# Kernel tuning notes

Measured on AMD Instinct MI355X. Metric: run time of the kernel, lower is better.

Reference implementation:

```python
import jax, jax.numpy as jnp
import numpy as np

NUM_STATES = 16
NUM_CHAINS = 8
NUM_NODES = 5000
NUM_ITERS = 100


def setup_inputs() -> dict:
    key = jax.random.key(0)
    k1, k2, k3, k4 = jax.random.split(key, 4)
    return {
        "unnormalized_state_init": jax.random.normal(k1, (NUM_STATES,), dtype=jnp.float32),
        "unnormalized_chain_weights": jax.random.normal(k2, (1, NUM_NODES, NUM_CHAINS), dtype=jnp.float32),
        "unnormalized_emission_matrix": jax.random.normal(k3, (NUM_STATES, NUM_NODES), dtype=jnp.float32),
        "unnormalized_transition_matrix": jax.random.normal(k4, (NUM_STATES, NUM_STATES), dtype=jnp.float32),
    }


def reference(unnormalized_state_init, unnormalized_chain_weights,
              unnormalized_emission_matrix, unnormalized_transition_matrix):
    T = NUM_ITERS
    # log_transform_params: row-stochastic normalizations in log space
    log_state_init = jax.nn.log_softmax(unnormalized_state_init)                    # (S,)
    log_chain_weights = jax.nn.log_softmax(unnormalized_chain_weights, axis=-1)     # (1,N,C)
    log_emission = jax.nn.log_softmax(unnormalized_emission_matrix, axis=1)         # (S,N)
    log_transition = jax.nn.log_softmax(unnormalized_transition_matrix, axis=1)     # (S,S), rows P(next|prev)

    # log_weights: (S,N,C) = log P(node|state) + log P(chain|node,state)
    log_weights = log_emission[:, :, None] + log_chain_weights

    # HMM forward recursion on hidden-state marginals: h_t[j] = logsumexp_i(h_{t-1}[i] + logT[i,j])
    def step(h, _):
        h_new = jax.scipy.special.logsumexp(h[:, None] + log_transition, axis=0)
        return h_new, h_new

    _, hs = jax.lax.scan(step, log_state_init, None, length=T - 1)
    log_hidden_state_probs = jnp.concatenate([log_state_init[None], hs], axis=0)    # (T,S)

    # (T,S,N,C): broadcast hidden-state marginal into node/chain weights
    log_observed_state_probs_ = log_weights[None] + log_hidden_state_probs[:, :, None, None]

    # logsumexp over states (axis 1) then chains (axis -1) == joint logsumexp over axes (1,3)
    log_observed_state_probs = jax.scipy.special.logsumexp(log_observed_state_probs_, axis=(1, 3))  # (T,N)

    # permute(0,1,3,2): (T,S,C,N)
    log_observed_state_probs_perm = jnp.transpose(log_observed_state_probs_, (0, 1, 3, 2))

    return (log_observed_state_probs, log_observed_state_probs_perm, log_hidden_state_probs)
```

## Files before the change

### kernel.cpp

```cpp
#include <hip/hip_runtime.h>
#include <math.h>

#define S 16
#define C 8
#define N 5000
#define T 100
#define N4 1250

__global__ __launch_bounds__(256) void prep_kernel(const float* __restrict__ u_init,
                                                   const float* __restrict__ u_cw,
                                                   const float* __restrict__ u_e,
                                                   const float* __restrict__ u_T,
                                                   float* __restrict__ ws_le,
                                                   float* __restrict__ ws_lcw,
                                                   float* __restrict__ ws_h,
                                                   float* __restrict__ out_h) {
    const int b = blockIdx.x;
    const int tid = threadIdx.x;

    if (b < 16) {
        const float* row = u_e + b * N;
        __shared__ float red[256];
        float m = -INFINITY;
        for (int n = tid; n < N; n += 256) m = fmaxf(m, row[n]);
        red[tid] = m;
        __syncthreads();
        for (int o = 128; o > 0; o >>= 1) {
            if (tid < o) red[tid] = fmaxf(red[tid], red[tid + o]);
            __syncthreads();
        }
        m = red[0];
        __syncthreads();
        float sum = 0.f;
        for (int n = tid; n < N; n += 256) sum += expf(row[n] - m);
        red[tid] = sum;
        __syncthreads();
        for (int o = 128; o > 0; o >>= 1) {
            if (tid < o) red[tid] += red[tid + o];
            __syncthreads();
        }
        const float lse = m + logf(red[0]);
        for (int n = tid; n < N; n += 256) ws_le[b * N + n] = row[n] - lse;
    } else if (b < 36) {
        const int n = (b - 16) * 256 + tid;
        if (n < N) {
            float v[C];
            float m = -INFINITY;
            for (int c = 0; c < C; ++c) {
                v[c] = u_cw[n * C + c];
                m = fmaxf(m, v[c]);
            }
            float s = 0.f;
            for (int c = 0; c < C; ++c) s += expf(v[c] - m);
            const float lse = m + logf(s);
            for (int c = 0; c < C; ++c) ws_lcw[n * C + c] = v[c] - lse;
        }
    } else {
        if (tid < S) {
            const int j = tid;
            float m = -INFINITY;
            for (int i = 0; i < S; ++i) m = fmaxf(m, u_init[i]);
            float ssum = 0.f;
            for (int i = 0; i < S; ++i) ssum += expf(u_init[i] - m);
            const float lse0 = m + logf(ssum);
            const float h0 = u_init[j] - lse0;
            out_h[j] = h0;
            ws_h[j] = h0;
            float mr = -INFINITY;
            for (int k = 0; k < S; ++k) mr = fmaxf(mr, u_T[j * S + k]);
            float sr = 0.f;
            for (int k = 0; k < S; ++k) sr += expf(u_T[j * S + k] - mr);
            const float lse_row = mr + logf(sr);
            float texp[S];
            #pragma unroll
            for (int i = 0; i < S; ++i) {
                const float lse_i = __shfl(lse_row, i, 64);
                texp[i] = expf(u_T[i * S + j] - lse_i);
            }
            float p = expf(h0);
            for (int t = 1; t < T; ++t) {
                float pn = 0.f;
                #pragma unroll
                for (int i = 0; i < S; ++i) {
                    pn = fmaf(__shfl(p, i, 64), texp[i], pn);
                }
                p = pn;
                const float hv = logf(p);
                out_h[t * S + j] = hv;
                ws_h[t * S + j] = hv;
            }
        }
    }
}

__global__ __launch_bounds__(256) void main_kernel(const float* __restrict__ ws_le,
                                                   const float* __restrict__ ws_lcw,
                                                   const float* __restrict__ ws_h,
                                                   float* __restrict__ out0,
                                                   float* __restrict__ out_perm) {
    const int t = blockIdx.y;
    const int i = blockIdx.x * 256 + threadIdx.x;

    __shared__ float h[S];
    if (threadIdx.x < S) h[threadIdx.x] = ws_h[t * S + threadIdx.x];
    __syncthreads();
    if (i >= N4) return;

    float lc[C][4];
    const float4* __restrict__ lcw4 = (const float4*)ws_lcw;
    #pragma unroll
    for (int j = 0; j < 8; ++j) {
        const float4 v = lcw4[8 * (size_t)i + j];
        const int nl = j >> 1;
        const int cb = (j & 1) * 4;
        lc[cb + 0][nl] = v.x;
        lc[cb + 1][nl] = v.y;
        lc[cb + 2][nl] = v.z;
        lc[cb + 3][nl] = v.w;
    }

    const float4* __restrict__ le4 = (const float4*)ws_le;
    float4* __restrict__ outp4 = (float4*)out_perm;

    float4 a[S];
    float4 m4 = make_float4(-INFINITY, -INFINITY, -INFINITY, -INFINITY);

    #pragma unroll
    for (int s = 0; s < S; ++s) {
        const float4 e = le4[(size_t)s * N4 + i];
        const float hs = h[s];
        a[s].x = e.x + hs; a[s].y = e.y + hs; a[s].z = e.z + hs; a[s].w = e.w + hs;
        m4.x = fmaxf(m4.x, a[s].x); m4.y = fmaxf(m4.y, a[s].y);
        m4.z = fmaxf(m4.z, a[s].z); m4.w = fmaxf(m4.w, a[s].w);
        const size_t base = (((size_t)t * S + s) * C) * N4 + i;
        #pragma unroll
        for (int c = 0; c < C; ++c) {
            float4 w;
            w.x = a[s].x + lc[c][0];
            w.y = a[s].y + lc[c][1];
            w.z = a[s].z + lc[c][2];
            w.w = a[s].w + lc[c][3];
            outp4[base + (size_t)c * N4] = w;
        }
    }

    float4 sum4 = make_float4(0.f, 0.f, 0.f, 0.f);
    #pragma unroll
    for (int s = 0; s < S; ++s) {
        sum4.x += expf(a[s].x - m4.x);
        sum4.y += expf(a[s].y - m4.y);
        sum4.z += expf(a[s].z - m4.z);
        sum4.w += expf(a[s].w - m4.w);
    }
    float4 r;
    r.x = m4.x + logf(sum4.x);
    r.y = m4.y + logf(sum4.y);
    r.z = m4.z + logf(sum4.z);
    r.w = m4.w + logf(sum4.w);
    ((float4*)out0)[(size_t)t * N4 + i] = r;
}

extern "C" void kernel_launch(void* const* d_in, const int* in_sizes, int n_in,
                              void* d_out, int out_size, void* d_ws, size_t ws_size,
                              hipStream_t stream) {
    const float* u_init = (const float*)d_in[0];
    const float* u_cw   = (const float*)d_in[1];
    const float* u_e    = (const float*)d_in[2];
    const float* u_T    = (const float*)d_in[3];

    float* out = (float*)d_out;
    float* out0     = out;
    float* out_perm = out + (size_t)T * N;
    float* out_h    = out + (size_t)T * N + (size_t)T * S * C * N;

    float* ws  = (float*)d_ws;
    float* ws_h   = ws;
    float* ws_le  = ws + 1600;
    float* ws_lcw = ws + 1600 + 80000;

    prep_kernel<<<37, 256, 0, stream>>>(u_init, u_cw, u_e, u_T, ws_le, ws_lcw, ws_h, out_h);
    main_kernel<<<dim3(5, T), 256, 0, stream>>>(ws_le, ws_lcw, ws_h, out0, out_perm);
}
```

Baseline: 284.7 us.

## Split main kernel into per-state perm kernel and separate logsumexp kernel

The fused main kernel, which ran one thread per 4 nodes over all 16 states, is split into two kernels. The permuted-output kernel now runs over a (node, state, time) grid, giving 16x more blocks, and writes with nontemporal stores. A separate kernel computes the logsumexp output. The aim is to raise parallelism and memory-level concurrency for the dominant 51 MB write stream, at the cost of one extra launch and re-reading the small emission and chain-weight arrays for each state.

```diff
diff --git a/kernel.cpp b/kernel.cpp
--- a/kernel.cpp
+++ b/kernel.cpp
@@ -6,6 +6,8 @@
 #define N 5000
 #define T 100
 #define N4 1250
+
+typedef float vfloat4 __attribute__((ext_vector_type(4)));
 
 __global__ __launch_bounds__(256) void prep_kernel(const float* __restrict__ u_init,
                                                    const float* __restrict__ u_cw,
@@ -93,24 +95,23 @@
     }
 }
 
-__global__ __launch_bounds__(256) void main_kernel(const float* __restrict__ ws_le,
-                                                   const float* __restrict__ ws_lcw,
+__global__ __launch_bounds__(256) void perm_kernel(const vfloat4* __restrict__ le4,
+                                                   const vfloat4* __restrict__ lcw4,
                                                    const float* __restrict__ ws_h,
-                                                   float* __restrict__ out0,
-                                                   float* __restrict__ out_perm) {
-    const int t = blockIdx.y;
+                                                   vfloat4* __restrict__ outp4) {
     const int i = blockIdx.x * 256 + threadIdx.x;
-
-    __shared__ float h[S];
-    if (threadIdx.x < S) h[threadIdx.x] = ws_h[t * S + threadIdx.x];
-    __syncthreads();
+    const int s = blockIdx.y;
+    const int t = blockIdx.z;
     if (i >= N4) return;
 
+    const float hval = ws_h[t * S + s];
+    const vfloat4 e = le4[(size_t)s * N4 + i];
+    const vfloat4 a = e + hval;
+
     float lc[C][4];
-    const float4* __restrict__ lcw4 = (const float4*)ws_lcw;
     #pragma unroll
     for (int j = 0; j < 8; ++j) {
-        const float4 v = lcw4[8 * (size_t)i + j];
+        const vfloat4 v = lcw4[8 * (size_t)i + j];
         const int nl = j >> 1;
         const int cb = (j & 1) * 4;
         lc[cb + 0][nl] = v.x;
@@ -119,32 +120,38 @@
         lc[cb + 3][nl] = v.w;
     }
 
-    const float4* __restrict__ le4 = (const float4*)ws_le;
-    float4* __restrict__ outp4 = (float4*)out_perm;
+    const size_t base = (((size_t)t * S + s) * C) * N4 + i;
+    #pragma unroll
+    for (int c = 0; c < C; ++c) {
+        vfloat4 w;
+        w.x = a.x + lc[c][0];
+        w.y = a.y + lc[c][1];
+        w.z = a.z + lc[c][2];
+        w.w = a.w + lc[c][3];
+        __builtin_nontemporal_store(w, &outp4[base + (size_t)c * N4]);
+    }
+}
 
-    float4 a[S];
-    float4 m4 = make_float4(-INFINITY, -INFINITY, -INFINITY, -INFINITY);
+__global__ __launch_bounds__(256) void out0_kernel(const vfloat4* __restrict__ le4,
+                                                   const float* __restrict__ ws_h,
+                                                   vfloat4* __restrict__ out0_4) {
+    const int t = blockIdx.y;
+    const int i = blockIdx.x * 256 + threadIdx.x;
+    __shared__ float h[S];
+    if (threadIdx.x < S) h[threadIdx.x] = ws_h[t * S + threadIdx.x];
+    __syncthreads();
+    if (i >= N4) return;
 
+    vfloat4 a[S];
+    vfloat4 m4 = {-INFINITY, -INFINITY, -INFINITY, -INFINITY};
     #pragma unroll
     for (int s = 0; s < S; ++s) {
-        const float4 e = le4[(size_t)s * N4 + i];
-        const float hs = h[s];
-        a[s].x = e.x + hs; a[s].y = e.y + hs; a[s].z = e.z + hs; a[s].w = e.w + hs;
+        const vfloat4 e = le4[(size_t)s * N4 + i];
+        a[s] = e + h[s];
         m4.x = fmaxf(m4.x, a[s].x); m4.y = fmaxf(m4.y, a[s].y);
         m4.z = fmaxf(m4.z, a[s].z); m4.w = fmaxf(m4.w, a[s].w);
-        const size_t base = (((size_t)t * S + s) * C) * N4 + i;
-        #pragma unroll
-        for (int c = 0; c < C; ++c) {
-            float4 w;
-            w.x = a[s].x + lc[c][0];
-            w.y = a[s].y + lc[c][1];
-            w.z = a[s].z + lc[c][2];
-            w.w = a[s].w + lc[c][3];
-            outp4[base + (size_t)c * N4] = w;
-        }
     }
-
-    float4 sum4 = make_float4(0.f, 0.f, 0.f, 0.f);
+    vfloat4 sum4 = {0.f, 0.f, 0.f, 0.f};
     #pragma unroll
     for (int s = 0; s < S; ++s) {
         sum4.x += expf(a[s].x - m4.x);
@@ -152,12 +159,12 @@
         sum4.z += expf(a[s].z - m4.z);
         sum4.w += expf(a[s].w - m4.w);
     }
-    float4 r;
+    vfloat4 r;
     r.x = m4.x + logf(sum4.x);
     r.y = m4.y + logf(sum4.y);
     r.z = m4.z + logf(sum4.z);
     r.w = m4.w + logf(sum4.w);
-    ((float4*)out0)[(size_t)t * N4 + i] = r;
+    __builtin_nontemporal_store(r, &out0_4[(size_t)t * N4 + i]);
 }
 
 extern "C" void kernel_launch(void* const* d_in, const int* in_sizes, int n_in,
@@ -179,5 +186,7 @@
     float* ws_lcw = ws + 1600 + 80000;
 
     prep_kernel<<<37, 256, 0, stream>>>(u_init, u_cw, u_e, u_T, ws_le, ws_lcw, ws_h, out_h);
-    main_kernel<<<dim3(5, T), 256, 0, stream>>>(ws_le, ws_lcw, ws_h, out0, out_perm);
+    perm_kernel<<<dim3(5, S, T), 256, 0, stream>>>((const vfloat4*)ws_le, (const vfloat4*)ws_lcw,
+                                                   ws_h, (vfloat4*)out_perm);
+    out0_kernel<<<dim3(5, T), 256, 0, stream>>>((const vfloat4*)ws_le, ws_h, (vfloat4*)out0);
 }
```

Result: slower. 306.7 us (+7.7%).
